# Performance work log

Measured on AMD Instinct MI355X. Metric: run time of the kernel, lower is better.

## Reference

```python
import jax, jax.numpy as jnp
import numpy as np


def _dct_basis(n: int) -> jnp.ndarray:
    # Unnormalized DCT-II basis matching torch_dct.dct(norm=None):
    # X[k] = 2 * sum_n x[n] * cos(pi*(2n+1)*k / (2N))
    k = np.arange(n)[:, None]
    m = np.arange(n)[None, :]
    D = 2.0 * np.cos(np.pi * (2.0 * m + 1.0) * k / (2.0 * n))
    return jnp.asarray(D, dtype=jnp.float32)


def setup_inputs() -> dict:
    key = jax.random.key(0)
    img = jax.random.normal(key, (32, 3, 512, 512), dtype=jnp.float32)
    return {"img": img}


def reference(img) -> jnp.ndarray:
    B, C, H, W = img.shape
    Dh = _dct_basis(H)  # [H, H]
    Dw = _dct_basis(W)  # [W, W]
    x = img.astype(jnp.float32)
    # 2D DCT-II: Dh @ x @ Dw^T, batched over (B, C); fused /1000 scale.
    tmp = jnp.einsum('kh,bchw->bckw', Dh, x)
    out = jnp.einsum('bckw,lw->bckl', tmp, Dw) / 1000.0
    return out
```

## Files before the change

### kernel.cpp

```cpp
#include <hip/hip_runtime.h>
#include <hip/hip_bf16.h>
#include <stdint.h>

#define NPIX 512
#define NBC  96
#define NWG8 (NBC * 4)

typedef __attribute__((ext_vector_type(8))) short bf16x8;
typedef __attribute__((ext_vector_type(4))) float f32x4;
typedef __attribute__((ext_vector_type(8))) unsigned short u16x8;

__device__ __forceinline__ unsigned short f2bf(float f) {
    __hip_bfloat16 h = __float2bfloat16(f);
    union { __hip_bfloat16 h; unsigned short u; } v;
    v.h = h;
    return v.u;
}

#define GLD16(g, l) __builtin_amdgcn_global_load_lds( \
    (const __attribute__((address_space(1))) void*)(const void*)(g), \
    (__attribute__((address_space(3))) void*)(void*)(l), 16, 0, 0)

#define SBAR() do { __builtin_amdgcn_sched_barrier(0); \
                    __builtin_amdgcn_s_barrier(); \
                    __builtin_amdgcn_sched_barrier(0); } while (0)
#define LGKM0() do { asm volatile("s_waitcnt lgkmcnt(0)" ::: "memory"); \
                     __builtin_amdgcn_sched_barrier(0); } while (0)
#define SB0() __builtin_amdgcn_sched_barrier(0)
#define VMW(n) do { asm volatile("s_waitcnt vmcnt(" #n ")" ::: "memory"); } while (0)

__global__ void k_basis(unsigned short* __restrict__ D) {
    int idx = blockIdx.x * 256 + threadIdx.x;
    int k = idx >> 9, n = idx & 511;
    int m = ((2 * n + 1) * k) & 2047;
    float ang = (float)m * 3.06796157577128218e-03f;
    D[idx] = f2bf(2.0f * cosf(ang));
}

__global__ __launch_bounds__(512) void k_s1x(
        const unsigned short* __restrict__ D,
        const float* __restrict__ X,
        unsigned short* __restrict__ sT) {
    __shared__ __align__(16) char LDS[131072];

    const int bid = blockIdx.x;
    const int nb  = (bid & 7) * (NWG8 / 8) + (bid >> 3);
    const int bc = nb >> 2, mt = (nb >> 1) & 1, nt = nb & 1;
    const int mA0 = mt * 256, nB0 = nt * 256;
    const unsigned short* Aimg = D;
    const float* Bimg = X + (size_t)bc * NPIX * NPIX;

    const int tid  = threadIdx.x;
    const int lane = tid & 63;
    const int wid  = tid >> 6;
    const int wr = wid >> 2, wc = wid & 3;
    const int rm = lane & 15;
    const int kq = lane >> 4;

    f32x4 acc[8][4] = {};
    bf16x8 a[4], b0[2], b1[2];

    auto stageA = [&](int kt, int p2, int H) {
        int c = tid;
        int rp = c >> 2, g = c & 3;
        int gs = g ^ (rp & 3);
        int row = ((rp >> 6) << 7) + H * 64 + (rp & 63);
        GLD16(Aimg + (size_t)(mA0 + row) * NPIX + kt * 32 + gs * 8,
              LDS + p2 * 16384 + H * 8192 + c * 16);
    };
    auto stageB = [&](int kt, int s3, int H) {
        #pragma unroll
        for (int it = 0; it < 2; ++it) {
            int c = it * 512 + tid;
            int rp = c >> 3, g = c & 7;
            int gs = g ^ (rp & 7);
            int row = ((rp >> 5) << 6) + H * 32 + (rp & 31);
            GLD16(Bimg + (size_t)(nB0 + row) * NPIX + kt * 32 + gs * 4,
                  LDS + 32768 + s3 * 32768 + H * 16384 + c * 16);
        }
    };
    auto readA = [&](int p2, int mh) {
        const char* base = LDS + p2 * 16384 + mh * 8192;
        #pragma unroll
        for (int f = 0; f < 4; ++f) {
            int rp = wr * 64 + f * 16 + rm;
            int slot = kq ^ (rm & 3);
            a[f] = *(const bf16x8*)(base + rp * 64 + slot * 16);
        }
    };
    auto readB = [&](int s3, int nh, bf16x8 (&b)[2]) {
        const char* base = LDS + 32768 + s3 * 32768 + nh * 16384;
        #pragma unroll
        for (int jj = 0; jj < 2; ++jj) {
            int rp = wc * 32 + jj * 16 + rm;
            const char* rb = base + rp * 128;
            f32x4 v0 = *(const f32x4*)(rb + (((kq * 2 + 0) ^ (rm & 7)) * 16));
            f32x4 v1 = *(const f32x4*)(rb + (((kq * 2 + 1) ^ (rm & 7)) * 16));
            bf16x8 t;
            t[0] = (short)f2bf(v0[0]); t[1] = (short)f2bf(v0[1]);
            t[2] = (short)f2bf(v0[2]); t[3] = (short)f2bf(v0[3]);
            t[4] = (short)f2bf(v1[0]); t[5] = (short)f2bf(v1[1]);
            t[6] = (short)f2bf(v1[2]); t[7] = (short)f2bf(v1[3]);
            b[jj] = t;
        }
    };
    auto mma = [&](int mh, int nh, bf16x8 (&b)[2]) {
        __builtin_amdgcn_s_setprio(1);
        #pragma unroll
        for (int f = 0; f < 4; ++f)
            #pragma unroll
            for (int jj = 0; jj < 2; ++jj)
                acc[mh * 4 + f][nh * 2 + jj] = __builtin_amdgcn_mfma_f32_16x16x32_bf16(
                    a[f], b[jj], acc[mh * 4 + f][nh * 2 + jj], 0, 0, 0);
        __builtin_amdgcn_s_setprio(0);
    };

    stageB(0, 0, 0); SB0();
    stageB(0, 0, 1); SB0();
    stageA(0, 0, 0); SB0();
    stageB(1, 1, 0); SB0();
    stageB(1, 1, 1); SB0();
    stageA(0, 0, 1); SB0();

    for (int T = 0; T < 14; ++T) {
        const int p2 = T & 1, p2n = p2 ^ 1;
        const int s3 = T % 3, s3b = (T + 2) % 3;
        VMW(5); SBAR();
        readA(p2, 0); readB(s3, 0, b0);
        stageA(T + 1, p2n, 0); SB0();
        LGKM0(); mma(0, 0, b0);
        SBAR();
        readB(s3, 1, b1);
        stageB(T + 2, s3b, 0); SB0();
        LGKM0(); mma(0, 1, b1);
        VMW(3); SBAR();
        readA(p2, 1);
        stageB(T + 2, s3b, 1); SB0();
        LGKM0(); mma(1, 0, b0);
        SBAR();
        stageA(T + 1, p2n, 1); SB0();
        mma(1, 1, b1);
    }
    {
        VMW(5); SBAR();
        readA(0, 0); readB(2, 0, b0);
        stageA(15, 1, 0); SB0();
        LGKM0(); mma(0, 0, b0);
        SBAR();
        readB(2, 1, b1); LGKM0(); mma(0, 1, b1);
        VMW(1); SBAR();
        readA(0, 1); LGKM0(); mma(1, 0, b0);
        SBAR();
        stageA(15, 1, 1); SB0();
        mma(1, 1, b1);
    }
    {
        VMW(1); SBAR();
        readA(1, 0); readB(0, 0, b0); LGKM0(); mma(0, 0, b0);
        SBAR();
        readB(0, 1, b1); LGKM0(); mma(0, 1, b1);
        VMW(0); SBAR();
        readA(1, 1); LGKM0(); mma(1, 0, b0);
        SBAR();
        mma(1, 1, b1);
    }

    unsigned short* Co = sT + (size_t)bc * NPIX * NPIX;
    #pragma unroll
    for (int mh = 0; mh < 2; ++mh)
        #pragma unroll
        for (int f = 0; f < 4; ++f) {
            int l_ = mA0 + wr * 128 + mh * 64 + f * 16 + kq * 4;
            #pragma unroll
            for (int nh = 0; nh < 2; ++nh)
                #pragma unroll
                for (int jj = 0; jj < 2; ++jj) {
                    int h_ = nB0 + wc * 64 + (nh * 2 + jj) * 16 + rm;
                    f32x4 v = acc[mh * 4 + f][nh * 2 + jj];
                    #pragma unroll
                    for (int r = 0; r < 4; ++r)
                        Co[(size_t)(l_ + r) * NPIX + h_] = f2bf(v[r]);
                }
        }
}

__global__ __launch_bounds__(512) void k_s2g(
        const unsigned short* __restrict__ D,
        const unsigned short* __restrict__ sT,
        float* __restrict__ Cv) {
    __shared__ __align__(16) char LDS[131072];

    const int bid = blockIdx.x;
    const int nb  = (bid & 7) * (NWG8 / 8) + (bid >> 3);
    const int bc = nb >> 2, mt = (nb >> 1) & 1, nt = nb & 1;
    const int mA0 = mt * 256, nB0 = nt * 256;
    const unsigned short* Aimg = D;
    const unsigned short* Bimg = sT + (size_t)bc * NPIX * NPIX;

    const int tid  = threadIdx.x;
    const int lane = tid & 63;
    const int wid  = tid >> 6;
    const int wr = wid >> 2, wc = wid & 3;
    const int rm = lane & 15;
    const int kq = lane >> 4;

    f32x4 acc[8][4] = {};
    bf16x8 a[4][2], b0[2][2], b1[2][2];

    auto stageA = [&](int kt, int p, int H) {
        char* dst = LDS + p * 32768 + H * 16384;
        #pragma unroll
        for (int it = 0; it < 2; ++it) {
            int c = it * 512 + tid;
            int rp = c >> 3, g = c & 7;
            int gs = g ^ (rp & 7);
            int row = ((rp >> 6) << 7) + H * 64 + (rp & 63);
            GLD16(Aimg + (size_t)(mA0 + row) * NPIX + kt * 64 + gs * 8, dst + c * 16);
        }
    };
    auto stageB = [&](int kt, int p, int H) {
        char* dst = LDS + 65536 + p * 32768 + H * 16384;
        #pragma unroll
        for (int it = 0; it < 2; ++it) {
            int c = it * 512 + tid;
            int rp = c >> 3, g = c & 7;
            int gs = g ^ (rp & 7);
            int row = ((rp >> 5) << 6) + H * 32 + (rp & 31);
            GLD16(Bimg + (size_t)(nB0 + row) * NPIX + kt * 64 + gs * 8, dst + c * 16);
        }
    };
    auto readA = [&](int p, int mh) {
        const char* base = LDS + p * 32768 + mh * 16384;
        #pragma unroll
        for (int f = 0; f < 4; ++f) {
            int rp = wr * 64 + f * 16 + rm;
            #pragma unroll
            for (int ks = 0; ks < 2; ++ks) {
                int slot = (ks * 4 + kq) ^ (rm & 7);
                a[f][ks] = *(const bf16x8*)(base + rp * 128 + slot * 16);
            }
        }
    };
    auto readB = [&](int p, int nh, bf16x8 (&b)[2][2]) {
        const char* base = LDS + 65536 + p * 32768 + nh * 16384;
        #pragma unroll
        for (int jj = 0; jj < 2; ++jj) {
            int rp = wc * 32 + jj * 16 + rm;
            #pragma unroll
            for (int ks = 0; ks < 2; ++ks) {
                int slot = (ks * 4 + kq) ^ (rm & 7);
                b[jj][ks] = *(const bf16x8*)(base + rp * 128 + slot * 16);
            }
        }
    };
    auto mma = [&](int mh, int nh, bf16x8 (&b)[2][2]) {
        __builtin_amdgcn_s_setprio(1);
        #pragma unroll
        for (int f = 0; f < 4; ++f)
            #pragma unroll
            for (int jj = 0; jj < 2; ++jj)
                #pragma unroll
                for (int ks = 0; ks < 2; ++ks)
                    acc[mh * 4 + f][nh * 2 + jj] = __builtin_amdgcn_mfma_f32_16x16x32_bf16(
                        a[f][ks], b[jj][ks], acc[mh * 4 + f][nh * 2 + jj], 0, 0, 0);
        __builtin_amdgcn_s_setprio(0);
    };

    stageA(0, 0, 0); stageB(0, 0, 0); stageB(0, 0, 1); stageA(0, 0, 1);

    for (int T = 0; T < 7; ++T) {
        const int p = T & 1, pn = p ^ 1;
        asm volatile("s_waitcnt vmcnt(4)" ::: "memory"); SBAR();
        readA(p, 0); readB(p, 0, b0); stageA(T + 1, pn, 0);
        LGKM0(); mma(0, 0, b0);
        asm volatile("s_waitcnt vmcnt(4)" ::: "memory"); SBAR();
        readB(p, 1, b1); stageB(T + 1, pn, 0);
        LGKM0(); mma(0, 1, b1);
        asm volatile("s_waitcnt vmcnt(4)" ::: "memory"); SBAR();
        readA(p, 1); stageB(T + 1, pn, 1);
        LGKM0(); mma(1, 0, b0);
        SBAR();
        stageA(T + 1, pn, 1);
        mma(1, 1, b1);
    }
    {
        asm volatile("s_waitcnt vmcnt(4)" ::: "memory"); SBAR();
        readA(1, 0); readB(1, 0, b0); LGKM0(); mma(0, 0, b0);
        asm volatile("s_waitcnt vmcnt(2)" ::: "memory"); SBAR();
        readB(1, 1, b1); LGKM0(); mma(0, 1, b1);
        asm volatile("s_waitcnt vmcnt(0)" ::: "memory"); SBAR();
        readA(1, 1); LGKM0(); mma(1, 0, b0);
        SBAR();
        mma(1, 1, b1);
    }

    float* Co = Cv + (size_t)bc * NPIX * NPIX;
    #pragma unroll
    for (int mh = 0; mh < 2; ++mh)
        #pragma unroll
        for (int f = 0; f < 4; ++f) {
            int k_ = mA0 + wr * 128 + mh * 64 + f * 16 + kq * 4;
            #pragma unroll
            for (int nh = 0; nh < 2; ++nh)
                #pragma unroll
                for (int jj = 0; jj < 2; ++jj) {
                    int l_ = nB0 + wc * 64 + (nh * 2 + jj) * 16 + rm;
                    f32x4 v = acc[mh * 4 + f][nh * 2 + jj];
                    #pragma unroll
                    for (int r = 0; r < 4; ++r)
                        Co[(size_t)(k_ + r) * NPIX + l_] = v[r] * 1.0e-3f;
                }
        }
}

extern "C" void kernel_launch(void* const* d_in, const int* in_sizes, int n_in,
                              void* d_out, int out_size, void* d_ws, size_t ws_size,
                              hipStream_t stream) {
    const float* img = (const float*)d_in[0];
    float* out = (float*)d_out;

    unsigned short* D  = (unsigned short*)d_ws;
    unsigned short* sT = (unsigned short*)((char*)d_ws + 512 * 1024);

    k_basis<<<dim3(512 * 512 / 256), dim3(256), 0, stream>>>(D);

    k_s1x<<<dim3(NWG8), dim3(512), 0, stream>>>(D, img, sT);

    k_s2g<<<dim3(NWG8), dim3(512), 0, stream>>>(D, sT, out);
}
```

Baseline: 92.88 us.

## Halve stage-1 N tile to 128 and double workgroup count for occupancy

```diff
diff --git a/kernel.cpp b/kernel.cpp
--- a/kernel.cpp
+++ b/kernel.cpp
@@ -5,6 +5,7 @@
 #define NPIX 512
 #define NBC  96
 #define NWG8 (NBC * 4)
+#define NWG13 (NBC * 8)
 
 typedef __attribute__((ext_vector_type(8))) short bf16x8;
 typedef __attribute__((ext_vector_type(4))) float f32x4;
@@ -37,16 +38,16 @@
     D[idx] = f2bf(2.0f * cosf(ang));
 }
 
-__global__ __launch_bounds__(512) void k_s1x(
+__global__ __launch_bounds__(512, 4) void k_s1x(
         const unsigned short* __restrict__ D,
         const float* __restrict__ X,
         unsigned short* __restrict__ sT) {
-    __shared__ __align__(16) char LDS[131072];
+    __shared__ __align__(16) char LDS[81920];
 
     const int bid = blockIdx.x;
-    const int nb  = (bid & 7) * (NWG8 / 8) + (bid >> 3);
-    const int bc = nb >> 2, mt = (nb >> 1) & 1, nt = nb & 1;
-    const int mA0 = mt * 256, nB0 = nt * 256;
+    const int nb  = (bid & 7) * (NWG13 / 8) + (bid >> 3);
+    const int bc = nb >> 3, mt = (nb >> 2) & 1, nt = nb & 3;
+    const int mA0 = mt * 256, nB0 = nt * 128;
     const unsigned short* Aimg = D;
     const float* Bimg = X + (size_t)bc * NPIX * NPIX;
 
@@ -57,42 +58,39 @@
     const int rm = lane & 15;
     const int kq = lane >> 4;
 
-    f32x4 acc[8][4] = {};
-    bf16x8 a[4], b0[2], b1[2];
+    f32x4 acc[8][2] = {};
+    bf16x8 a[4], b[2];
 
     auto stageA = [&](int kt, int p2, int H) {
         int c = tid;
         int rp = c >> 2, g = c & 3;
-        int gs = g ^ (rp & 3);
+        int gs = g ^ ((rp >> 1) & 3);
         int row = ((rp >> 6) << 7) + H * 64 + (rp & 63);
         GLD16(Aimg + (size_t)(mA0 + row) * NPIX + kt * 32 + gs * 8,
               LDS + p2 * 16384 + H * 8192 + c * 16);
     };
     auto stageB = [&](int kt, int s3, int H) {
-        #pragma unroll
-        for (int it = 0; it < 2; ++it) {
-            int c = it * 512 + tid;
-            int rp = c >> 3, g = c & 7;
-            int gs = g ^ (rp & 7);
-            int row = ((rp >> 5) << 6) + H * 32 + (rp & 31);
-            GLD16(Bimg + (size_t)(nB0 + row) * NPIX + kt * 32 + gs * 4,
-                  LDS + 32768 + s3 * 32768 + H * 16384 + c * 16);
-        }
+        int c = tid;
+        int rp = c >> 3, g = c & 7;
+        int gs = g ^ (rp & 7);
+        int row = ((rp >> 5) << 6) + H * 32 + (rp & 31);
+        GLD16(Bimg + (size_t)(nB0 + row) * NPIX + kt * 32 + gs * 4,
+              LDS + 32768 + s3 * 16384 + H * 8192 + c * 16);
     };
     auto readA = [&](int p2, int mh) {
         const char* base = LDS + p2 * 16384 + mh * 8192;
         #pragma unroll
         for (int f = 0; f < 4; ++f) {
             int rp = wr * 64 + f * 16 + rm;
-            int slot = kq ^ (rm & 3);
+            int slot = kq ^ ((rm >> 1) & 3);
             a[f] = *(const bf16x8*)(base + rp * 64 + slot * 16);
         }
     };
-    auto readB = [&](int s3, int nh, bf16x8 (&b)[2]) {
-        const char* base = LDS + 32768 + s3 * 32768 + nh * 16384;
+    auto readB = [&](int s3) {
+        const char* base = LDS + 32768 + s3 * 16384 + (wc & 1) * 8192;
         #pragma unroll
         for (int jj = 0; jj < 2; ++jj) {
-            int rp = wc * 32 + jj * 16 + rm;
+            int rp = (wc >> 1) * 32 + jj * 16 + rm;
             const char* rb = base + rp * 128;
             f32x4 v0 = *(const f32x4*)(rb + (((kq * 2 + 0) ^ (rm & 7)) * 16));
             f32x4 v1 = *(const f32x4*)(rb + (((kq * 2 + 1) ^ (rm & 7)) * 16));
@@ -104,65 +102,55 @@
             b[jj] = t;
         }
     };
-    auto mma = [&](int mh, int nh, bf16x8 (&b)[2]) {
+    auto mma = [&](int mh) {
         __builtin_amdgcn_s_setprio(1);
         #pragma unroll
         for (int f = 0; f < 4; ++f)
             #pragma unroll
             for (int jj = 0; jj < 2; ++jj)
-                acc[mh * 4 + f][nh * 2 + jj] = __builtin_amdgcn_mfma_f32_16x16x32_bf16(
-                    a[f], b[jj], acc[mh * 4 + f][nh * 2 + jj], 0, 0, 0);
+                acc[mh * 4 + f][jj] = __builtin_amdgcn_mfma_f32_16x16x32_bf16(
+                    a[f], b[jj], acc[mh * 4 + f][jj], 0, 0, 0);
         __builtin_amdgcn_s_setprio(0);
     };
 
     stageB(0, 0, 0); SB0();
     stageB(0, 0, 1); SB0();
     stageA(0, 0, 0); SB0();
+    stageA(0, 0, 1); SB0();
     stageB(1, 1, 0); SB0();
     stageB(1, 1, 1); SB0();
-    stageA(0, 0, 1); SB0();
 
     for (int T = 0; T < 14; ++T) {
         const int p2 = T & 1, p2n = p2 ^ 1;
         const int s3 = T % 3, s3b = (T + 2) % 3;
-        VMW(5); SBAR();
-        readA(p2, 0); readB(s3, 0, b0);
+        VMW(3); SBAR();
+        readA(p2, 0); readB(s3);
         stageA(T + 1, p2n, 0); SB0();
-        LGKM0(); mma(0, 0, b0);
-        SBAR();
-        readB(s3, 1, b1);
         stageB(T + 2, s3b, 0); SB0();
-        LGKM0(); mma(0, 1, b1);
+        LGKM0(); mma(0);
         VMW(3); SBAR();
         readA(p2, 1);
+        stageA(T + 1, p2n, 1); SB0();
         stageB(T + 2, s3b, 1); SB0();
-        LGKM0(); mma(1, 0, b0);
-        SBAR();
-        stageA(T + 1, p2n, 1); SB0();
-        mma(1, 1, b1);
+        LGKM0(); mma(1);
     }
     {
-        VMW(5); SBAR();
-        readA(0, 0); readB(2, 0, b0);
+        VMW(3); SBAR();
+        readA(0, 0); readB(2);
         stageA(15, 1, 0); SB0();
-        LGKM0(); mma(0, 0, b0);
-        SBAR();
-        readB(2, 1, b1); LGKM0(); mma(0, 1, b1);
-        VMW(1); SBAR();
-        readA(0, 1); LGKM0(); mma(1, 0, b0);
-        SBAR();
+        LGKM0(); mma(0);
+        VMW(2); SBAR();
+        readA(0, 1);
         stageA(15, 1, 1); SB0();
-        mma(1, 1, b1);
+        LGKM0(); mma(1);
     }
     {
         VMW(1); SBAR();
-        readA(1, 0); readB(0, 0, b0); LGKM0(); mma(0, 0, b0);
-        SBAR();
-        readB(0, 1, b1); LGKM0(); mma(0, 1, b1);
+        readA(1, 0); readB(0);
+        LGKM0(); mma(0);
         VMW(0); SBAR();
-        readA(1, 1); LGKM0(); mma(1, 0, b0);
-        SBAR();
-        mma(1, 1, b1);
+        readA(1, 1);
+        LGKM0(); mma(1);
     }
 
     unsigned short* Co = sT + (size_t)bc * NPIX * NPIX;
@@ -172,15 +160,13 @@
         for (int f = 0; f < 4; ++f) {
             int l_ = mA0 + wr * 128 + mh * 64 + f * 16 + kq * 4;
             #pragma unroll
-            for (int nh = 0; nh < 2; ++nh)
+            for (int jj = 0; jj < 2; ++jj) {
+                int h_ = nB0 + wc * 32 + jj * 16 + rm;
+                f32x4 v = acc[mh * 4 + f][jj];
                 #pragma unroll
-                for (int jj = 0; jj < 2; ++jj) {
-                    int h_ = nB0 + wc * 64 + (nh * 2 + jj) * 16 + rm;
-                    f32x4 v = acc[mh * 4 + f][nh * 2 + jj];
-                    #pragma unroll
-                    for (int r = 0; r < 4; ++r)
-                        Co[(size_t)(l_ + r) * NPIX + h_] = f2bf(v[r]);
-                }
+                for (int r = 0; r < 4; ++r)
+                    Co[(size_t)(l_ + r) * NPIX + h_] = f2bf(v[r]);
+            }
         }
 }
 
@@ -324,7 +310,7 @@
 
     k_basis<<<dim3(512 * 512 / 256), dim3(256), 0, stream>>>(D);
 
-    k_s1x<<<dim3(NWG8), dim3(512), 0, stream>>>(D, img, sT);
+    k_s1x<<<dim3(NWG13), dim3(512), 0, stream>>>(D, img, sT);
 
     k_s2g<<<dim3(NWG8), dim3(512), 0, stream>>>(D, sT, out);
 }
```

Measured after the change: 84.39 us. 1.1x faster.
